# Kernel tuning notes

Hardware: AMD Instinct MI355X
Metric: run time of the kernel (lower is better)

Reference implementation:

```python
import jax, jax.numpy as jnp
import numpy as np

T = 2048           # tokens (single prefill sequence)
HIDDEN = 2048
H = 16             # num heads
D_NOPE = 128
D_ROPE = 64
D_V = 128
KV_LORA = 512
EPS = 1e-6
ROPE_THETA = 10000.0


def setup_inputs() -> dict:
    key = jax.random.key(0)
    ks = jax.random.split(key, 7)
    s = 0.02
    return {
        "positions": jnp.arange(T, dtype=jnp.int64) if jax.config.jax_enable_x64 else jnp.arange(T, dtype=jnp.int32),
        "hidden_states": jax.random.normal(ks[0], (T, HIDDEN), dtype=jnp.float32),
        "w_q": jax.random.normal(ks[1], (HIDDEN, H * (D_NOPE + D_ROPE)), dtype=jnp.float32) * s,
        "w_kv_a": jax.random.normal(ks[2], (HIDDEN, KV_LORA + D_ROPE), dtype=jnp.float32) * s,
        "kv_a_ln_w": jax.random.uniform(ks[3], (KV_LORA,), dtype=jnp.float32, minval=0.5, maxval=1.5),
        "w_kv_b": jax.random.normal(ks[4], (KV_LORA, H * (D_NOPE + D_V)), dtype=jnp.float32) * s,
        "w_o": jax.random.normal(ks[5], (H * D_V, HIDDEN), dtype=jnp.float32) * s,
    }


def _rms_norm(x, w):
    var = jnp.mean(jnp.square(x), axis=-1, keepdims=True)
    return x * jax.lax.rsqrt(var + EPS) * w


def _rope_nonneox(x, positions):
    # x: [..., D_ROPE], GPT-J (interleaved) style rotation
    inv_freq = 1.0 / (ROPE_THETA ** (jnp.arange(0, D_ROPE, 2, dtype=jnp.float32) / D_ROPE))
    freqs = positions.astype(jnp.float32)[:, None] * inv_freq  # [T, D_ROPE//2]
    cos, sin = jnp.cos(freqs), jnp.sin(freqs)
    # broadcast over head dim if present
    while cos.ndim < x.ndim:
        cos, sin = cos[:, None], sin[:, None]
    x1, x2 = x[..., 0::2], x[..., 1::2]
    o1 = x1 * cos - x2 * sin
    o2 = x2 * cos + x1 * sin
    return jnp.stack([o1, o2], axis=-1).reshape(x.shape)


def reference(positions, hidden_states, w_q, w_kv_a, kv_a_ln_w, w_kv_b, w_o):
    scaling = (D_NOPE + D_ROPE) ** -0.5
    # q projection (q_lora_rank is None branch)
    q = (hidden_states @ w_q).reshape(T, H, D_NOPE + D_ROPE)
    q_nope, q_pe = q[..., :D_NOPE], q[..., D_NOPE:]
    # compressed KV latent
    latent = hidden_states @ w_kv_a                 # [T, KV_LORA + D_ROPE]
    kv_a = _rms_norm(latent[:, :KV_LORA], kv_a_ln_w)
    k_pe = latent[:, KV_LORA:]                      # [T, D_ROPE], shared across heads
    # decompress to per-head k_nope and v (kv_b_proj)
    kv = (kv_a @ w_kv_b).reshape(T, H, D_NOPE + D_V)
    k_nope, v = kv[..., :D_NOPE], kv[..., D_NOPE:]
    # non-neox RoPE
    q_pe = _rope_nonneox(q_pe, positions)
    k_pe = _rope_nonneox(k_pe, positions)           # [T, D_ROPE]
    # concat rope parts (k_pe broadcast over heads)
    q_full = jnp.concatenate([q_nope, q_pe], axis=-1)                         # [T,H,192]
    k_full = jnp.concatenate([k_nope, jnp.broadcast_to(k_pe[:, None, :], (T, H, D_ROPE))], axis=-1)
    # causal MHA
    scores = jnp.einsum("qhd,khd->hqk", q_full, k_full) * scaling
    causal = positions[:, None] >= positions[None, :]
    scores = jnp.where(causal[None], scores, -jnp.inf)
    attn = jax.nn.softmax(scores, axis=-1)
    out = jnp.einsum("hqk,khd->qhd", attn, v).reshape(T, H * D_V)
    return out @ w_o
```

## Files before the change

### kernel.cpp

```cpp
#include <hip/hip_runtime.h>
#include <hip/hip_bf16.h>
#include <stdint.h>

#define T_SEQ   2048
#define NHEAD   16
#define NPAD1   3712

typedef short bf16x8 __attribute__((ext_vector_type(8)));
typedef float f32x4  __attribute__((ext_vector_type(4)));

__device__ __forceinline__ unsigned short f2bf(float f) {
  union { float f; uint32_t u; } v; v.f = f;
  uint32_t u = v.u;
  uint32_t r = u + 0x7FFF + ((u >> 16) & 1);
  return (unsigned short)(r >> 16);
}

__device__ __forceinline__ void async16(const void* g, void* l) {
  __builtin_amdgcn_global_load_lds(
      (const __attribute__((address_space(1))) void*)g,
      (__attribute__((address_space(3))) void*)l, 16, 0, 0);
}

__global__ __launch_bounds__(256) void convert_bf16_kernel(
    const float* __restrict__ in, unsigned short* __restrict__ out, int n) {
  int i = (blockIdx.x * 256 + threadIdx.x) * 4;
  if (i + 3 < n) {
    float4 v = *(const float4*)(in + i);
    ushort4 o;
    o.x = f2bf(v.x); o.y = f2bf(v.y); o.z = f2bf(v.z); o.w = f2bf(v.w);
    *(ushort4*)(out + i) = o;
  }
}

__global__ __launch_bounds__(256) void transpose_bf16_kernel(
    const float* __restrict__ in, unsigned short* __restrict__ out, int R, int C) {
  __shared__ float tile[32][33];
  int r0 = blockIdx.x * 32, c0 = blockIdx.y * 32;
  int tx = threadIdx.x & 31, ty = threadIdx.x >> 5;
  for (int i = 0; i < 4; i++)
    tile[ty + i * 8][tx] = in[(size_t)(r0 + ty + i * 8) * C + c0 + tx];
  __syncthreads();
  for (int i = 0; i < 4; i++) {
    int c = ty + i * 8;
    out[(size_t)(c0 + c) * R + r0 + tx] = f2bf(tile[tx][c]);
  }
}

template<int OUT_BF16>
__global__ __launch_bounds__(256) void gemm_bt_kernel(
    const unsigned short* __restrict__ A, const unsigned short* __restrict__ B,
    void* __restrict__ Cv, int M, int N, int K) {
  __shared__ __align__(16) unsigned short Asm[2][128 * 32];
  __shared__ __align__(16) unsigned short Bsm[2][128 * 32];
  int tid = threadIdx.x, wid = tid >> 6, lane = tid & 63;
  int lrow = lane & 15, lquad = lane >> 4;
  int m0 = blockIdx.x * 128, n0 = blockIdx.y * 128;
  int wm = (wid & 1) * 64, wn = (wid >> 1) * 64;

  int row_s = tid >> 2, cc_s = tid & 3;
  const unsigned short* Ag0 = A + (size_t)(m0 + row_s) * K + cc_s * 8;
  const unsigned short* Ag1 = A + (size_t)(m0 + row_s + 64) * K + cc_s * 8;
  const unsigned short* Bg0 = B + (size_t)(n0 + row_s) * K + cc_s * 8;
  const unsigned short* Bg1 = B + (size_t)(n0 + row_s + 64) * K + cc_s * 8;

  f32x4 acc[4][4];
  for (int i = 0; i < 4; i++) for (int j = 0; j < 4; j++) acc[i][j] = (f32x4){0.f,0.f,0.f,0.f};

  async16(Ag0, &Asm[0][tid * 8]);
  async16(Ag1, &Asm[0][2048 + tid * 8]);
  async16(Bg0, &Bsm[0][tid * 8]);
  async16(Bg1, &Bsm[0][2048 + tid * 8]);

  int cur = 0;
  for (int k0 = 0; k0 < K; k0 += 32) {
    __syncthreads();
    if (k0 + 32 < K) {
      int nxt = cur ^ 1, kk = k0 + 32;
      async16(Ag0 + kk, &Asm[nxt][tid * 8]);
      async16(Ag1 + kk, &Asm[nxt][2048 + tid * 8]);
      async16(Bg0 + kk, &Bsm[nxt][tid * 8]);
      async16(Bg1 + kk, &Bsm[nxt][2048 + tid * 8]);
    }
    const unsigned short* As = Asm[cur];
    const unsigned short* Bs = Bsm[cur];
    bf16x8 af[4], bfr[4];
    for (int mt = 0; mt < 4; mt++)
      af[mt] = *(const bf16x8*)(As + (wm + mt * 16 + lrow) * 32 + lquad * 8);
    for (int nt = 0; nt < 4; nt++)
      bfr[nt] = *(const bf16x8*)(Bs + (wn + nt * 16 + lrow) * 32 + lquad * 8);
    for (int mt = 0; mt < 4; mt++)
      for (int nt = 0; nt < 4; nt++)
        acc[mt][nt] = __builtin_amdgcn_mfma_f32_16x16x32_bf16(af[mt], bfr[nt], acc[mt][nt], 0, 0, 0);
    cur ^= 1;
  }
  for (int mt = 0; mt < 4; mt++)
    for (int nt = 0; nt < 4; nt++) {
      int row = m0 + wm + mt * 16 + lquad * 4;
      int col = n0 + wn + nt * 16 + lrow;
      for (int r = 0; r < 4; r++) {
        if (OUT_BF16)
          ((unsigned short*)Cv)[(size_t)(row + r) * N + col] = f2bf(acc[mt][nt][r]);
        else
          ((float*)Cv)[(size_t)(row + r) * N + col] = acc[mt][nt][r];
      }
    }
}

__global__ __launch_bounds__(256) void postproc1_kernel(
    const float* __restrict__ q_lat,
    const float* __restrict__ ln_w,
    const int* __restrict__ positions,
    unsigned short* __restrict__ kv_a,
    unsigned short* __restrict__ q_full,
    unsigned short* __restrict__ k_pe)
{
  int t = blockIdx.x, tid = threadIdx.x;
  const float* row = q_lat + (size_t)t * NPAD1;
  const float scaling = 0.07216878364870323f;

  float v0 = row[3072 + tid], v1 = row[3072 + 256 + tid];
  float ss = v0 * v0 + v1 * v1;
  for (int m = 1; m < 64; m <<= 1) ss += __shfl_xor(ss, m, 64);
  __shared__ float red[4];
  if ((tid & 63) == 0) red[tid >> 6] = ss;
  __shared__ float kro[64];
  float pos = (float)positions[t];
  if (tid < 32) {
    float inv_freq = powf(10000.f, -(float)(2 * tid) / 64.f);
    float c, s; sincosf(pos * inv_freq, &s, &c);
    float x1 = row[3584 + 2 * tid], x2 = row[3584 + 2 * tid + 1];
    kro[2 * tid]     = x1 * c - x2 * s;
    kro[2 * tid + 1] = x2 * c + x1 * s;
  }
  __syncthreads();
  float rstd = rsqrtf((red[0] + red[1] + red[2] + red[3]) * (1.f / 512.f) + 1e-6f);
  kv_a[(size_t)t * 512 + tid]       = f2bf(v0 * rstd * ln_w[tid]);
  kv_a[(size_t)t * 512 + 256 + tid] = f2bf(v1 * rstd * ln_w[256 + tid]);
  if (tid < 64) k_pe[(size_t)t * 64 + tid] = f2bf(kro[tid]);

  for (int i = tid; i < NHEAD * 128; i += 256) {
    int h = i >> 7, d = i & 127;
    q_full[((size_t)h * T_SEQ + t) * 192 + d] = f2bf(row[h * 192 + d] * scaling);
  }
  for (int i = tid; i < NHEAD * 32; i += 256) {
    int h = i >> 5, p = i & 31;
    float inv_freq = powf(10000.f, -(float)(2 * p) / 64.f);
    float c, s; sincosf(pos * inv_freq, &s, &c);
    float x1 = row[h * 192 + 128 + 2 * p], x2 = row[h * 192 + 128 + 2 * p + 1];
    q_full[((size_t)h * T_SEQ + t) * 192 + 128 + 2 * p]     = f2bf((x1 * c - x2 * s) * scaling);
    q_full[((size_t)h * T_SEQ + t) * 192 + 128 + 2 * p + 1] = f2bf((x2 * c + x1 * s) * scaling);
  }
}

__global__ __launch_bounds__(256) void kpack_kernel(
    const unsigned short* __restrict__ kv_b,
    const unsigned short* __restrict__ k_pe,
    unsigned short* __restrict__ k_full) {
  int idx = blockIdx.x * 256 + threadIdx.x;
  int cc = idx % 24, rest = idx / 24;
  int t = rest & (T_SEQ - 1), h = rest >> 11;
  uint4 v = (cc < 16)
      ? *(const uint4*)(kv_b + (size_t)t * 4096 + h * 256 + cc * 8)
      : *(const uint4*)(k_pe + (size_t)t * 64 + (cc - 16) * 8);
  *(uint4*)(k_full + (size_t)idx * 8) = v;
}

__global__ __launch_bounds__(256) void vtrans_kernel(
    const unsigned short* __restrict__ kv_b, unsigned short* __restrict__ v_t) {
  __shared__ unsigned short tile[32][41];
  int h = blockIdx.z, t0 = blockIdx.x * 32, d0 = blockIdx.y * 32;
  int tx = threadIdx.x & 31, ty = threadIdx.x >> 5;
  for (int i = 0; i < 4; i++)
    tile[ty + i * 8][tx] = kv_b[(size_t)(t0 + ty + i * 8) * 4096 + h * 256 + 128 + d0 + tx];
  __syncthreads();
  for (int i = 0; i < 4; i++)
    v_t[((size_t)h * 128 + d0 + ty + i * 8) * T_SEQ + t0 + tx] = tile[tx][ty + i * 8];
}

#define PP 72
__global__ __launch_bounds__(256, 2) void flash_kernel(
    const unsigned short* __restrict__ q_full,
    const unsigned short* __restrict__ k_full,
    const unsigned short* __restrict__ v_t,
    unsigned short* __restrict__ attn_out)
{
  __shared__ __align__(16) unsigned short Ksm[2][1536 * 8];
  __shared__ __align__(16) unsigned short Vsm[1024 * 8];
  __shared__ __align__(16) unsigned short Psm[4][16 * PP];
  int h = blockIdx.x;
  int y = blockIdx.y;
  int qb = (y < 16) ? (31 - y) : (y - 16);
  int tid = threadIdx.x, wid = tid >> 6, lane = tid & 63;
  int lrow = lane & 15, lquad = lane >> 4;
  int x7 = lrow & 7;

  const unsigned short* kh = k_full + (size_t)h * T_SEQ * 192;
  const unsigned short* vh = v_t    + (size_t)h * 128 * T_SEQ;

  int gK[6], gV[4];
  #pragma unroll
  for (int j = 0; j < 6; j++) {
    int s = tid + j * 256, row = s / 24, cm = s - row * 24;
    gK[j] = row * 192 + (cm ^ (row & 7)) * 8;
  }
  #pragma unroll
  for (int j = 0; j < 4; j++) {
    int s = tid + j * 256, d = s >> 3;
    gV[j] = d * T_SEQ + ((s & 7) ^ (d & 7)) * 8;
  }
  int kx[6], vx[2];
  #pragma unroll
  for (int kc = 0; kc < 6; kc++) kx[kc] = ((kc * 4 + lquad) ^ x7) * 8 + lrow * 24 * 8;
  #pragma unroll
  for (int kc = 0; kc < 2; kc++) vx[kc] = ((kc * 4 + lquad) ^ x7) * 8 + lrow * 8 * 8;

  bf16x8 qf[6];
  {
    const unsigned short* qrow =
        q_full + ((size_t)h * T_SEQ + qb * 64 + wid * 16 + lrow) * 192 + lquad * 8;
    #pragma unroll
    for (int kc = 0; kc < 6; kc++) qf[kc] = *(const bf16x8*)(qrow + kc * 32);
  }
  f32x4 oacc[8];
  for (int i = 0; i < 8; i++) oacc[i] = (f32x4){0.f,0.f,0.f,0.f};
  float lsum[4] = {0.f, 0.f, 0.f, 0.f};
  int q_row_g = qb * 64 + wid * 16 + lquad * 4;
  unsigned short* pw = &Psm[wid][0];

  #pragma unroll
  for (int j = 0; j < 6; j++) async16(kh + gK[j], &Ksm[0][(tid + j * 256) * 8]);

  int cur = 0;
  for (int kb = 0; kb <= qb; kb++) {
    __syncthreads();
    {
      const unsigned short* vb = vh + kb * 64;
      #pragma unroll
      for (int j = 0; j < 4; j++) async16(vb + gV[j], &Vsm[(tid + j * 256) * 8]);
    }
    const unsigned short* Ks = Ksm[cur];
    f32x4 sacc[4];
    #pragma unroll
    for (int nt = 0; nt < 4; nt++) {
      sacc[nt] = (f32x4){0.f,0.f,0.f,0.f};
      #pragma unroll
      for (int kc = 0; kc < 6; kc++) {
        bf16x8 kf = *(const bf16x8*)(Ks + nt * 384 * 8 + kx[kc]);
        sacc[nt] = __builtin_amdgcn_mfma_f32_16x16x32_bf16(qf[kc], kf, sacc[nt], 0, 0, 0);
      }
    }
    __syncthreads();
    if (kb < qb) {
      const unsigned short* kb1 = kh + (size_t)(kb + 1) * 64 * 192;
      #pragma unroll
      for (int j = 0; j < 6; j++) async16(kb1 + gK[j], &Ksm[cur ^ 1][(tid + j * 256) * 8]);
    }

    if (kb == qb) {
      int col_base = kb * 64;
      #pragma unroll
      for (int nt = 0; nt < 4; nt++) {
        int col = col_base + nt * 16 + lrow;
        #pragma unroll
        for (int r = 0; r < 4; r++)
          if (col > q_row_g + r) sacc[nt][r] = -1e30f;
      }
    }
    #pragma unroll
    for (int nt = 0; nt < 4; nt++)
      #pragma unroll
      for (int r = 0; r < 4; r++) {
        float p = __expf(sacc[nt][r]);
        sacc[nt][r] = p;
        lsum[r] += p;
      }

    #pragma unroll
    for (int nt = 0; nt < 4; nt++)
      #pragma unroll
      for (int r = 0; r < 4; r++)
        pw[(lquad * 4 + r) * PP + nt * 16 + lrow] = f2bf(sacc[nt][r]);

    #pragma unroll
    for (int kc = 0; kc < 2; kc++) {
      bf16x8 pf = *(const bf16x8*)(pw + lrow * PP + kc * 32 + lquad * 8);
      #pragma unroll
      for (int ntv = 0; ntv < 8; ntv++) {
        bf16x8 vf = *(const bf16x8*)(Vsm + ntv * 128 * 8 + vx[kc]);
        oacc[ntv] = __builtin_amdgcn_mfma_f32_16x16x32_bf16(pf, vf, oacc[ntv], 0, 0, 0);
      }
    }
    cur ^= 1;
  }

  #pragma unroll
  for (int r = 0; r < 4; r++) {
    float s = lsum[r];
    s += __shfl_xor(s, 1, 64);
    s += __shfl_xor(s, 2, 64);
    s += __shfl_xor(s, 4, 64);
    s += __shfl_xor(s, 8, 64);
    lsum[r] = 1.f / s;
  }
  for (int r = 0; r < 4; r++) {
    int row = qb * 64 + wid * 16 + lquad * 4 + r;
    for (int ntv = 0; ntv < 8; ntv++)
      attn_out[(size_t)row * 2048 + h * 128 + ntv * 16 + lrow] = f2bf(oacc[ntv][r] * lsum[r]);
  }
}

extern "C" void kernel_launch(void* const* d_in, const int* in_sizes, int n_in,
                              void* d_out, int out_size, void* d_ws, size_t ws_size,
                              hipStream_t stream) {
  const int*   positions = (const int*)d_in[0];
  const float* hs     = (const float*)d_in[1];
  const float* w_q    = (const float*)d_in[2];
  const float* w_kv_a = (const float*)d_in[3];
  const float* ln_w   = (const float*)d_in[4];
  const float* w_kv_b = (const float*)d_in[5];
  const float* w_o    = (const float*)d_in[6];
  float* out = (float*)d_out;

  char* ws = (char*)d_ws;
  size_t off = 0;
  auto alloc = [&](size_t bytes) { void* p = ws + off; off += (bytes + 255) & ~(size_t)255; return p; };
  unsigned short* hs_bf   = (unsigned short*)alloc((size_t)2048 * 2048 * 2);
  unsigned short* wcat_t  = (unsigned short*)alloc((size_t)NPAD1 * 2048 * 2);
  float*          q_lat   = (float*)alloc((size_t)2048 * NPAD1 * 4);
  unsigned short* kv_a_bf = (unsigned short*)alloc((size_t)2048 * 512 * 2);
  unsigned short* wkvb_t  = (unsigned short*)alloc((size_t)4096 * 512 * 2);
  unsigned short* kv_b    = (unsigned short*)alloc((size_t)2048 * 4096 * 2);
  unsigned short* q_full  = (unsigned short*)alloc((size_t)NHEAD * 2048 * 192 * 2);
  unsigned short* k_pe    = (unsigned short*)alloc((size_t)2048 * 64 * 2);
  unsigned short* k_full  = (unsigned short*)alloc((size_t)NHEAD * 2048 * 192 * 2);
  unsigned short* v_t     = (unsigned short*)alloc((size_t)NHEAD * 128 * 2048 * 2);
  unsigned short* attn_o  = (unsigned short*)alloc((size_t)2048 * 2048 * 2);
  unsigned short* wo_t    = (unsigned short*)alloc((size_t)2048 * 2048 * 2);

  convert_bf16_kernel<<<4096, 256, 0, stream>>>(hs, hs_bf, 2048 * 2048);
  transpose_bf16_kernel<<<dim3(64, 96),  256, 0, stream>>>(w_q,    wcat_t,                       2048, 3072);
  transpose_bf16_kernel<<<dim3(64, 18),  256, 0, stream>>>(w_kv_a, wcat_t + (size_t)3072 * 2048, 2048, 576);
  transpose_bf16_kernel<<<dim3(16, 128), 256, 0, stream>>>(w_kv_b, wkvb_t,                       512,  4096);
  transpose_bf16_kernel<<<dim3(64, 64),  256, 0, stream>>>(w_o,    wo_t,                         2048, 2048);
  hipMemsetAsync(wcat_t + (size_t)3648 * 2048, 0, (size_t)64 * 2048 * 2, stream);

  gemm_bt_kernel<0><<<dim3(16, 29), 256, 0, stream>>>(hs_bf, wcat_t, q_lat, 2048, NPAD1, 2048);
  postproc1_kernel<<<2048, 256, 0, stream>>>(q_lat, ln_w, positions, kv_a_bf, q_full, k_pe);
  gemm_bt_kernel<1><<<dim3(16, 32), 256, 0, stream>>>(kv_a_bf, wkvb_t, kv_b, 2048, 4096, 512);
  kpack_kernel<<<3072, 256, 0, stream>>>(kv_b, k_pe, k_full);
  vtrans_kernel<<<dim3(64, 4, 16), 256, 0, stream>>>(kv_b, v_t);
  flash_kernel<<<dim3(16, 32), 256, 0, stream>>>(q_full, k_full, v_t, attn_o);
  gemm_bt_kernel<0><<<dim3(16, 16), 256, 0, stream>>>(attn_o, wo_t, out, 2048, 2048, 2048);
}
```

Baseline: 312.4 us.

## Fuse prep kernels, switch flash attention to 32x32 MFMA, smaller output GEMM tile

Merges the bf16 conversion, the weight transposes and the memset into one prep kernel, and merges kpack and vtrans into one kvpost kernel, which cuts launch count. The flash kernel is restructured around 32x32x16 MFMA: each wave handles a 32x32 score tile, P is shared through one block-wide LDS buffer, and row sums are reduced across waves via LDS. Postproc caches the RoPE sin/cos instead of recomputing them per head, and the output GEMM uses a 64-row M tile to launch more blocks. The risks are extra block syncs and LDS traffic in flash, and lower per-block reuse in the smaller GEMM tile.

```diff
diff --git a/kernel.cpp b/kernel.cpp
--- a/kernel.cpp
+++ b/kernel.cpp
@@ -6,8 +6,9 @@
 #define NHEAD   16
 #define NPAD1   3712
 
-typedef short bf16x8 __attribute__((ext_vector_type(8)));
-typedef float f32x4  __attribute__((ext_vector_type(4)));
+typedef short bf16x8  __attribute__((ext_vector_type(8)));
+typedef float f32x4   __attribute__((ext_vector_type(4)));
+typedef float f32x16  __attribute__((ext_vector_type(16)));
 
 __device__ __forceinline__ unsigned short f2bf(float f) {
   union { float f; uint32_t u; } v; v.f = f;
@@ -22,22 +23,11 @@
       (__attribute__((address_space(3))) void*)l, 16, 0, 0);
 }
 
-__global__ __launch_bounds__(256) void convert_bf16_kernel(
-    const float* __restrict__ in, unsigned short* __restrict__ out, int n) {
-  int i = (blockIdx.x * 256 + threadIdx.x) * 4;
-  if (i + 3 < n) {
-    float4 v = *(const float4*)(in + i);
-    ushort4 o;
-    o.x = f2bf(v.x); o.y = f2bf(v.y); o.z = f2bf(v.z); o.w = f2bf(v.w);
-    *(ushort4*)(out + i) = o;
-  }
-}
-
-__global__ __launch_bounds__(256) void transpose_bf16_kernel(
-    const float* __restrict__ in, unsigned short* __restrict__ out, int R, int C) {
-  __shared__ float tile[32][33];
-  int r0 = blockIdx.x * 32, c0 = blockIdx.y * 32;
-  int tx = threadIdx.x & 31, ty = threadIdx.x >> 5;
+__device__ __forceinline__ void tr32(const float* __restrict__ in,
+    unsigned short* __restrict__ out, int R, int C, int bx, int by,
+    float (*tile)[33], int tid) {
+  int r0 = bx * 32, c0 = by * 32;
+  int tx = tid & 31, ty = tid >> 5;
   for (int i = 0; i < 4; i++)
     tile[ty + i * 8][tx] = in[(size_t)(r0 + ty + i * 8) * C + c0 + tx];
   __syncthreads();
@@ -47,16 +37,49 @@
   }
 }
 
-template<int OUT_BF16>
+__global__ __launch_bounds__(256) void prep_kernel(
+    const float* __restrict__ hs, const float* __restrict__ w_q,
+    const float* __restrict__ w_kv_a, const float* __restrict__ w_kv_b,
+    const float* __restrict__ w_o,
+    unsigned short* __restrict__ hs_bf, unsigned short* __restrict__ wcat_t,
+    unsigned short* __restrict__ wkvb_t, unsigned short* __restrict__ wo_t) {
+  __shared__ float tile[32][33];
+  int bid = blockIdx.x, tid = threadIdx.x;
+  if (bid < 4096) {
+    int i = (bid * 256 + tid) * 4;
+    float4 v = *(const float4*)(hs + i);
+    ushort4 o; o.x = f2bf(v.x); o.y = f2bf(v.y); o.z = f2bf(v.z); o.w = f2bf(v.w);
+    *(ushort4*)(hs_bf + i) = o;
+  } else if (bid < 4096 + 6144) {
+    int l = bid - 4096;
+    tr32(w_q, wcat_t, 2048, 3072, l & 63, l >> 6, tile, tid);
+  } else if (bid < 4096 + 6144 + 1152) {
+    int l = bid - (4096 + 6144);
+    tr32(w_kv_a, wcat_t + (size_t)3072 * 2048, 2048, 576, l & 63, l >> 6, tile, tid);
+  } else if (bid < 4096 + 6144 + 1152 + 2048) {
+    int l = bid - (4096 + 6144 + 1152);
+    tr32(w_kv_b, wkvb_t, 512, 4096, l & 15, l >> 4, tile, tid);
+  } else if (bid < 4096 + 6144 + 1152 + 2048 + 4096) {
+    int l = bid - (4096 + 6144 + 1152 + 2048);
+    tr32(w_o, wo_t, 2048, 2048, l & 63, l >> 6, tile, tid);
+  } else {
+    int l = bid - (4096 + 6144 + 1152 + 2048 + 4096);
+    uint4 z = (uint4){0, 0, 0, 0};
+    *(uint4*)(wcat_t + (size_t)3648 * 2048 + (size_t)(l * 256 + tid) * 8) = z;
+  }
+}
+
+template<int TM, int OUT_BF16>
 __global__ __launch_bounds__(256) void gemm_bt_kernel(
     const unsigned short* __restrict__ A, const unsigned short* __restrict__ B,
     void* __restrict__ Cv, int M, int N, int K) {
-  __shared__ __align__(16) unsigned short Asm[2][128 * 32];
+  constexpr int MT = TM / 32;
+  __shared__ __align__(16) unsigned short Asm[2][TM * 32];
   __shared__ __align__(16) unsigned short Bsm[2][128 * 32];
   int tid = threadIdx.x, wid = tid >> 6, lane = tid & 63;
   int lrow = lane & 15, lquad = lane >> 4;
-  int m0 = blockIdx.x * 128, n0 = blockIdx.y * 128;
-  int wm = (wid & 1) * 64, wn = (wid >> 1) * 64;
+  int m0 = blockIdx.x * TM, n0 = blockIdx.y * 128;
+  int wm = (wid & 1) * (TM / 2), wn = (wid >> 1) * 64;
 
   int row_s = tid >> 2, cc_s = tid & 3;
   const unsigned short* Ag0 = A + (size_t)(m0 + row_s) * K + cc_s * 8;
@@ -64,11 +87,11 @@
   const unsigned short* Bg0 = B + (size_t)(n0 + row_s) * K + cc_s * 8;
   const unsigned short* Bg1 = B + (size_t)(n0 + row_s + 64) * K + cc_s * 8;
 
-  f32x4 acc[4][4];
-  for (int i = 0; i < 4; i++) for (int j = 0; j < 4; j++) acc[i][j] = (f32x4){0.f,0.f,0.f,0.f};
+  f32x4 acc[MT][4];
+  for (int i = 0; i < MT; i++) for (int j = 0; j < 4; j++) acc[i][j] = (f32x4){0.f,0.f,0.f,0.f};
 
   async16(Ag0, &Asm[0][tid * 8]);
-  async16(Ag1, &Asm[0][2048 + tid * 8]);
+  if (TM == 128) async16(Ag1, &Asm[0][2048 + tid * 8]);
   async16(Bg0, &Bsm[0][tid * 8]);
   async16(Bg1, &Bsm[0][2048 + tid * 8]);
 
@@ -78,23 +101,23 @@
     if (k0 + 32 < K) {
       int nxt = cur ^ 1, kk = k0 + 32;
       async16(Ag0 + kk, &Asm[nxt][tid * 8]);
-      async16(Ag1 + kk, &Asm[nxt][2048 + tid * 8]);
+      if (TM == 128) async16(Ag1 + kk, &Asm[nxt][2048 + tid * 8]);
       async16(Bg0 + kk, &Bsm[nxt][tid * 8]);
       async16(Bg1 + kk, &Bsm[nxt][2048 + tid * 8]);
     }
     const unsigned short* As = Asm[cur];
     const unsigned short* Bs = Bsm[cur];
-    bf16x8 af[4], bfr[4];
-    for (int mt = 0; mt < 4; mt++)
+    bf16x8 af[MT], bfr[4];
+    for (int mt = 0; mt < MT; mt++)
       af[mt] = *(const bf16x8*)(As + (wm + mt * 16 + lrow) * 32 + lquad * 8);
     for (int nt = 0; nt < 4; nt++)
       bfr[nt] = *(const bf16x8*)(Bs + (wn + nt * 16 + lrow) * 32 + lquad * 8);
-    for (int mt = 0; mt < 4; mt++)
+    for (int mt = 0; mt < MT; mt++)
       for (int nt = 0; nt < 4; nt++)
         acc[mt][nt] = __builtin_amdgcn_mfma_f32_16x16x32_bf16(af[mt], bfr[nt], acc[mt][nt], 0, 0, 0);
     cur ^= 1;
   }
-  for (int mt = 0; mt < 4; mt++)
+  for (int mt = 0; mt < MT; mt++)
     for (int nt = 0; nt < 4; nt++) {
       int row = m0 + wm + mt * 16 + lquad * 4;
       int col = n0 + wn + nt * 16 + lrow;
@@ -124,11 +147,12 @@
   for (int m = 1; m < 64; m <<= 1) ss += __shfl_xor(ss, m, 64);
   __shared__ float red[4];
   if ((tid & 63) == 0) red[tid >> 6] = ss;
-  __shared__ float kro[64];
+  __shared__ float kro[64], cf[32], sf[32];
   float pos = (float)positions[t];
   if (tid < 32) {
     float inv_freq = powf(10000.f, -(float)(2 * tid) / 64.f);
     float c, s; sincosf(pos * inv_freq, &s, &c);
+    cf[tid] = c; sf[tid] = s;
     float x1 = row[3584 + 2 * tid], x2 = row[3584 + 2 * tid + 1];
     kro[2 * tid]     = x1 * c - x2 * s;
     kro[2 * tid + 1] = x2 * c + x1 * s;
@@ -145,40 +169,41 @@
   }
   for (int i = tid; i < NHEAD * 32; i += 256) {
     int h = i >> 5, p = i & 31;
-    float inv_freq = powf(10000.f, -(float)(2 * p) / 64.f);
-    float c, s; sincosf(pos * inv_freq, &s, &c);
+    float c = cf[p], s = sf[p];
     float x1 = row[h * 192 + 128 + 2 * p], x2 = row[h * 192 + 128 + 2 * p + 1];
     q_full[((size_t)h * T_SEQ + t) * 192 + 128 + 2 * p]     = f2bf((x1 * c - x2 * s) * scaling);
     q_full[((size_t)h * T_SEQ + t) * 192 + 128 + 2 * p + 1] = f2bf((x2 * c + x1 * s) * scaling);
   }
 }
 
-__global__ __launch_bounds__(256) void kpack_kernel(
+__global__ __launch_bounds__(256) void kvpost_kernel(
     const unsigned short* __restrict__ kv_b,
     const unsigned short* __restrict__ k_pe,
-    unsigned short* __restrict__ k_full) {
-  int idx = blockIdx.x * 256 + threadIdx.x;
-  int cc = idx % 24, rest = idx / 24;
-  int t = rest & (T_SEQ - 1), h = rest >> 11;
-  uint4 v = (cc < 16)
-      ? *(const uint4*)(kv_b + (size_t)t * 4096 + h * 256 + cc * 8)
-      : *(const uint4*)(k_pe + (size_t)t * 64 + (cc - 16) * 8);
-  *(uint4*)(k_full + (size_t)idx * 8) = v;
-}
-
-__global__ __launch_bounds__(256) void vtrans_kernel(
-    const unsigned short* __restrict__ kv_b, unsigned short* __restrict__ v_t) {
+    unsigned short* __restrict__ k_full,
+    unsigned short* __restrict__ v_t) {
   __shared__ unsigned short tile[32][41];
-  int h = blockIdx.z, t0 = blockIdx.x * 32, d0 = blockIdx.y * 32;
-  int tx = threadIdx.x & 31, ty = threadIdx.x >> 5;
-  for (int i = 0; i < 4; i++)
-    tile[ty + i * 8][tx] = kv_b[(size_t)(t0 + ty + i * 8) * 4096 + h * 256 + 128 + d0 + tx];
-  __syncthreads();
-  for (int i = 0; i < 4; i++)
-    v_t[((size_t)h * 128 + d0 + ty + i * 8) * T_SEQ + t0 + tx] = tile[tx][ty + i * 8];
-}
-
-#define PP 72
+  int bid = blockIdx.x, tid = threadIdx.x;
+  if (bid < 3072) {
+    int idx = bid * 256 + tid;
+    int cc = idx % 24, rest = idx / 24;
+    int t = rest & (T_SEQ - 1), h = rest >> 11;
+    uint4 v = (cc < 16)
+        ? *(const uint4*)(kv_b + (size_t)t * 4096 + h * 256 + cc * 8)
+        : *(const uint4*)(k_pe + (size_t)t * 64 + (cc - 16) * 8);
+    *(uint4*)(k_full + (size_t)idx * 8) = v;
+  } else {
+    int l = bid - 3072;
+    int h = l >> 8, t0 = (l & 63) * 32, d0 = ((l >> 6) & 3) * 32;
+    int tx = tid & 31, ty = tid >> 5;
+    for (int i = 0; i < 4; i++)
+      tile[ty + i * 8][tx] = kv_b[(size_t)(t0 + ty + i * 8) * 4096 + h * 256 + 128 + d0 + tx];
+    __syncthreads();
+    for (int i = 0; i < 4; i++)
+      v_t[((size_t)h * 128 + d0 + ty + i * 8) * T_SEQ + t0 + tx] = tile[tx][ty + i * 8];
+  }
+}
+
+#define PP 76
 __global__ __launch_bounds__(256, 2) void flash_kernel(
     const unsigned short* __restrict__ q_full,
     const unsigned short* __restrict__ k_full,
@@ -187,13 +212,14 @@
 {
   __shared__ __align__(16) unsigned short Ksm[2][1536 * 8];
   __shared__ __align__(16) unsigned short Vsm[1024 * 8];
-  __shared__ __align__(16) unsigned short Psm[4][16 * PP];
+  __shared__ __align__(16) unsigned short Psm[64 * PP];
+  __shared__ float Lred[2][64];
   int h = blockIdx.x;
   int y = blockIdx.y;
   int qb = (y < 16) ? (31 - y) : (y - 16);
   int tid = threadIdx.x, wid = tid >> 6, lane = tid & 63;
-  int lrow = lane & 15, lquad = lane >> 4;
-  int x7 = lrow & 7;
+  int l31 = lane & 31, l5 = lane >> 5, x7 = l31 & 7;
+  int rq = wid & 1, kq = wid >> 1;
 
   const unsigned short* kh = k_full + (size_t)h * T_SEQ * 192;
   const unsigned short* vh = v_t    + (size_t)h * 128 * T_SEQ;
@@ -209,24 +235,29 @@
     int s = tid + j * 256, d = s >> 3;
     gV[j] = d * T_SEQ + ((s & 7) ^ (d & 7)) * 8;
   }
-  int kx[6], vx[2];
-  #pragma unroll
-  for (int kc = 0; kc < 6; kc++) kx[kc] = ((kc * 4 + lquad) ^ x7) * 8 + lrow * 24 * 8;
-  #pragma unroll
-  for (int kc = 0; kc < 2; kc++) vx[kc] = ((kc * 4 + lquad) ^ x7) * 8 + lrow * 8 * 8;
-
-  bf16x8 qf[6];
+  int kxo[12];
+  #pragma unroll
+  for (int kc = 0; kc < 12; kc++)
+    kxo[kc] = (kq * 32 + l31) * 192 + ((kc * 2 + l5) ^ x7) * 8;
+  int vxb[2];
+  #pragma unroll
+  for (int ntv = 0; ntv < 2; ntv++) vxb[ntv] = (kq * 64 + ntv * 32 + l31) * 64;
+
+  bf16x8 qf[12];
   {
     const unsigned short* qrow =
-        q_full + ((size_t)h * T_SEQ + qb * 64 + wid * 16 + lrow) * 192 + lquad * 8;
-    #pragma unroll
-    for (int kc = 0; kc < 6; kc++) qf[kc] = *(const bf16x8*)(qrow + kc * 32);
-  }
-  f32x4 oacc[8];
-  for (int i = 0; i < 8; i++) oacc[i] = (f32x4){0.f,0.f,0.f,0.f};
-  float lsum[4] = {0.f, 0.f, 0.f, 0.f};
-  int q_row_g = qb * 64 + wid * 16 + lquad * 4;
-  unsigned short* pw = &Psm[wid][0];
+        q_full + ((size_t)h * T_SEQ + qb * 64 + rq * 32 + l31) * 192 + l5 * 8;
+    #pragma unroll
+    for (int kc = 0; kc < 12; kc++) qf[kc] = *(const bf16x8*)(qrow + kc * 16);
+  }
+  f32x16 oacc[2];
+  for (int i = 0; i < 2; i++) oacc[i] = (f32x16)(0.f);
+  float lsum[16];
+  #pragma unroll
+  for (int r = 0; r < 16; r++) lsum[r] = 0.f;
+  int rl[16];
+  #pragma unroll
+  for (int r = 0; r < 16; r++) rl[r] = (r & 3) + 8 * (r >> 2) + 4 * l5;
 
   #pragma unroll
   for (int j = 0; j < 6; j++) async16(kh + gK[j], &Ksm[0][(tid + j * 256) * 8]);
@@ -240,73 +271,69 @@
       for (int j = 0; j < 4; j++) async16(vb + gV[j], &Vsm[(tid + j * 256) * 8]);
     }
     const unsigned short* Ks = Ksm[cur];
-    f32x4 sacc[4];
-    #pragma unroll
-    for (int nt = 0; nt < 4; nt++) {
-      sacc[nt] = (f32x4){0.f,0.f,0.f,0.f};
+    f32x16 sacc = (f32x16)(0.f);
+    #pragma unroll
+    for (int kc = 0; kc < 12; kc++) {
+      bf16x8 kf = *(const bf16x8*)(Ks + kxo[kc]);
+      sacc = __builtin_amdgcn_mfma_f32_32x32x16_bf16(qf[kc], kf, sacc, 0, 0, 0);
+    }
+    if (kb == qb) {
+      int col_g = kb * 64 + kq * 32 + l31;
+      int row_b = qb * 64 + rq * 32;
       #pragma unroll
-      for (int kc = 0; kc < 6; kc++) {
-        bf16x8 kf = *(const bf16x8*)(Ks + nt * 384 * 8 + kx[kc]);
-        sacc[nt] = __builtin_amdgcn_mfma_f32_16x16x32_bf16(qf[kc], kf, sacc[nt], 0, 0, 0);
-      }
-    }
+      for (int r = 0; r < 16; r++)
+        if (col_g > row_b + rl[r]) sacc[r] = -1e30f;
+    }
+    #pragma unroll
+    for (int r = 0; r < 16; r++) {
+      float p = __expf(sacc[r]);
+      sacc[r] = p;
+      lsum[r] += p;
+    }
+    #pragma unroll
+    for (int r = 0; r < 16; r++)
+      Psm[(rq * 32 + rl[r]) * PP + kq * 32 + l31] = f2bf(sacc[r]);
     __syncthreads();
     if (kb < qb) {
       const unsigned short* kb1 = kh + (size_t)(kb + 1) * 64 * 192;
       #pragma unroll
       for (int j = 0; j < 6; j++) async16(kb1 + gK[j], &Ksm[cur ^ 1][(tid + j * 256) * 8]);
     }
-
-    if (kb == qb) {
-      int col_base = kb * 64;
+    #pragma unroll
+    for (int kc = 0; kc < 4; kc++) {
+      bf16x8 pf = *(const bf16x8*)(Psm + (rq * 32 + l31) * PP + kc * 16 + l5 * 8);
       #pragma unroll
-      for (int nt = 0; nt < 4; nt++) {
-        int col = col_base + nt * 16 + lrow;
-        #pragma unroll
-        for (int r = 0; r < 4; r++)
-          if (col > q_row_g + r) sacc[nt][r] = -1e30f;
+      for (int ntv = 0; ntv < 2; ntv++) {
+        bf16x8 vf = *(const bf16x8*)(Vsm + vxb[ntv] + ((kc * 2 + l5) ^ x7) * 8);
+        oacc[ntv] = __builtin_amdgcn_mfma_f32_32x32x16_bf16(pf, vf, oacc[ntv], 0, 0, 0);
       }
     }
-    #pragma unroll
-    for (int nt = 0; nt < 4; nt++)
-      #pragma unroll
-      for (int r = 0; r < 4; r++) {
-        float p = __expf(sacc[nt][r]);
-        sacc[nt][r] = p;
-        lsum[r] += p;
-      }
-
-    #pragma unroll
-    for (int nt = 0; nt < 4; nt++)
-      #pragma unroll
-      for (int r = 0; r < 4; r++)
-        pw[(lquad * 4 + r) * PP + nt * 16 + lrow] = f2bf(sacc[nt][r]);
-
-    #pragma unroll
-    for (int kc = 0; kc < 2; kc++) {
-      bf16x8 pf = *(const bf16x8*)(pw + lrow * PP + kc * 32 + lquad * 8);
-      #pragma unroll
-      for (int ntv = 0; ntv < 8; ntv++) {
-        bf16x8 vf = *(const bf16x8*)(Vsm + ntv * 128 * 8 + vx[kc]);
-        oacc[ntv] = __builtin_amdgcn_mfma_f32_16x16x32_bf16(pf, vf, oacc[ntv], 0, 0, 0);
-      }
-    }
     cur ^= 1;
   }
 
   #pragma unroll
-  for (int r = 0; r < 4; r++) {
+  for (int r = 0; r < 16; r++) {
     float s = lsum[r];
     s += __shfl_xor(s, 1, 64);
     s += __shfl_xor(s, 2, 64);
     s += __shfl_xor(s, 4, 64);
     s += __shfl_xor(s, 8, 64);
-    lsum[r] = 1.f / s;
-  }
-  for (int r = 0; r < 4; r++) {
-    int row = qb * 64 + wid * 16 + lquad * 4 + r;
-    for (int ntv = 0; ntv < 8; ntv++)
-      attn_out[(size_t)row * 2048 + h * 128 + ntv * 16 + lrow] = f2bf(oacc[ntv][r] * lsum[r]);
+    s += __shfl_xor(s, 16, 64);
+    lsum[r] = s;
+  }
+  if (l31 == 0)
+    #pragma unroll
+    for (int r = 0; r < 16; r++) Lred[kq][rq * 32 + rl[r]] = lsum[r];
+  __syncthreads();
+  #pragma unroll
+  for (int r = 0; r < 16; r++) {
+    int row_l = rq * 32 + rl[r];
+    float inv = 1.f / (Lred[0][row_l] + Lred[1][row_l]);
+    int row_g = qb * 64 + row_l;
+    #pragma unroll
+    for (int ntv = 0; ntv < 2; ntv++)
+      attn_out[(size_t)row_g * 2048 + h * 128 + kq * 64 + ntv * 32 + l31] =
+          f2bf(oacc[ntv][r] * inv);
   }
 }
 
@@ -338,18 +365,12 @@
   unsigned short* attn_o  = (unsigned short*)alloc((size_t)2048 * 2048 * 2);
   unsigned short* wo_t    = (unsigned short*)alloc((size_t)2048 * 2048 * 2);
 
-  convert_bf16_kernel<<<4096, 256, 0, stream>>>(hs, hs_bf, 2048 * 2048);
-  transpose_bf16_kernel<<<dim3(64, 96),  256, 0, stream>>>(w_q,    wcat_t,                       2048, 3072);
-  transpose_bf16_kernel<<<dim3(64, 18),  256, 0, stream>>>(w_kv_a, wcat_t + (size_t)3072 * 2048, 2048, 576);
-  transpose_bf16_kernel<<<dim3(16, 128), 256, 0, stream>>>(w_kv_b, wkvb_t,                       512,  4096);
-  transpose_bf16_kernel<<<dim3(64, 64),  256, 0, stream>>>(w_o,    wo_t,                         2048, 2048);
-  hipMemsetAsync(wcat_t + (size_t)3648 * 2048, 0, (size_t)64 * 2048 * 2, stream);
-
-  gemm_bt_kernel<0><<<dim3(16, 29), 256, 0, stream>>>(hs_bf, wcat_t, q_lat, 2048, NPAD1, 2048);
+  prep_kernel<<<17600, 256, 0, stream>>>(hs, w_q, w_kv_a, w_kv_b, w_o,
+                                         hs_bf, wcat_t, wkvb_t, wo_t);
+  gemm_bt_kernel<128, 0><<<dim3(16, 29), 256, 0, stream>>>(hs_bf, wcat_t, q_lat, 2048, NPAD1, 2048);
   postproc1_kernel<<<2048, 256, 0, stream>>>(q_lat, ln_w, positions, kv_a_bf, q_full, k_pe);
-  gemm_bt_kernel<1><<<dim3(16, 32), 256, 0, stream>>>(kv_a_bf, wkvb_t, kv_b, 2048, 4096, 512);
-  kpack_kernel<<<3072, 256, 0, stream>>>(kv_b, k_pe, k_full);
-  vtrans_kernel<<<dim3(64, 4, 16), 256, 0, stream>>>(kv_b, v_t);
+  gemm_bt_kernel<128, 1><<<dim3(16, 32), 256, 0, stream>>>(kv_a_bf, wkvb_t, kv_b, 2048, 4096, 512);
+  kvpost_kernel<<<7168, 256, 0, stream>>>(kv_b, k_pe, k_full, v_t);
   flash_kernel<<<dim3(16, 32), 256, 0, stream>>>(q_full, k_full, v_t, attn_o);
-  gemm_bt_kernel<0><<<dim3(16, 16), 256, 0, stream>>>(attn_o, wo_t, out, 2048, 2048, 2048);
-}
+  gemm_bt_kernel<64, 0><<<dim3(32, 16), 256, 0, stream>>>(attn_o, wo_t, out, 2048, 2048, 2048);
+}
```

Result: faster. 280.6 us (-10.2%).
